# Optimization experiments

Measured on AMD Instinct MI355X. Metric: run time of the kernel, lower is better.

The kernel has to match this reference:

```python
import jax, jax.numpy as jnp
import numpy as np

INPUT_DIM = 512
NUM_CLASSES = 1000


def setup_inputs() -> dict:
    key = jax.random.key(0)
    kx, kw, kb = jax.random.split(key, 3)
    x = jax.random.normal(kx, (16384, INPUT_DIM), dtype=jnp.float32)
    # Stacked per-class Linear(input_dim, 2) params: W [C, 2, D], b [C, 2]
    lim = 1.0 / np.sqrt(INPUT_DIM)
    W = jax.random.uniform(kw, (NUM_CLASSES, 2, INPUT_DIM), dtype=jnp.float32, minval=-lim, maxval=lim)
    b = jax.random.uniform(kb, (NUM_CLASSES, 2), dtype=jnp.float32, minval=-lim, maxval=lim)
    return {"x": x, "W": W, "b": b}


def reference(x, W, b):
    # logits[b, c, t] = x[b, :] @ W[c, t, :] + b[c, t]
    logits = jnp.einsum("bd,ctd->bct", x, W) + b[None, :, :]  # [B, C, 2]
    # LogSoftmax over the 2 logits per class (torch dim=1 of the [B,2] slice)
    return jax.nn.log_softmax(logits, axis=-1)
```

## Files before the change

### kernel.cpp

```cpp
#include <hip/hip_runtime.h>
#include <cstdint>
#include <cstddef>

typedef unsigned short u16;
typedef unsigned int u32;
typedef __bf16 bf16x8 __attribute__((ext_vector_type(8)));
typedef float f32x4 __attribute__((ext_vector_type(4)));
typedef float f32x2 __attribute__((ext_vector_type(2)));

#define M_TOT 16384
#define C_TOT 1000
#define N_PAD 1024
#define K_TOT 512
#define OUT_STRIDE 2000
#define BM 128
#define BN 128
#define BK 32
#define NT 16
#define NWG 1024

__device__ __forceinline__ u16 f2bf(float f) {
  u32 u = __float_as_uint(f);
  u = (u + 0x7FFFu + ((u >> 16) & 1u)) >> 16;
  return (u16)u;
}

__global__ __launch_bounds__(256) void prep_kernel(const float* __restrict__ x,
                                                   const float* __restrict__ W,
                                                   const float* __restrict__ b,
                                                   u16* __restrict__ xb,
                                                   u16* __restrict__ wd,
                                                   float* __restrict__ bd) {
  if (blockIdx.x < 4096) {
    const int i = blockIdx.x * 256 + threadIdx.x;
    const float4* s = (const float4*)x;
    float4 a = s[2 * i], c = s[2 * i + 1];
    ushort4 r0, r1;
    r0.x = f2bf(a.x); r0.y = f2bf(a.y); r0.z = f2bf(a.z); r0.w = f2bf(a.w);
    r1.x = f2bf(c.x); r1.y = f2bf(c.y); r1.z = f2bf(c.z); r1.w = f2bf(c.w);
    ushort4* d = (ushort4*)xb;
    d[2 * i] = r0;
    d[2 * i + 1] = r1;
  } else {
    const int i = (blockIdx.x - 4096) * 256 + threadIdx.x;
    const int c = i >> 6;
    const int seg = i & 63;
    ushort4 r0 = {0, 0, 0, 0}, r1 = {0, 0, 0, 0};
    if (c < C_TOT) {
      const float4* w0 = (const float4*)(W + (size_t)(2 * c) * K_TOT) + seg * 2;
      const float4* w1 = (const float4*)(W + (size_t)(2 * c + 1) * K_TOT) + seg * 2;
      float4 a0 = w0[0], a1 = w0[1], c0 = w1[0], c1 = w1[1];
      r0.x = f2bf(a0.x - c0.x); r0.y = f2bf(a0.y - c0.y);
      r0.z = f2bf(a0.z - c0.z); r0.w = f2bf(a0.w - c0.w);
      r1.x = f2bf(a1.x - c1.x); r1.y = f2bf(a1.y - c1.y);
      r1.z = f2bf(a1.z - c1.z); r1.w = f2bf(a1.w - c1.w);
      if (seg == 0) bd[c] = b[2 * c] - b[2 * c + 1];
    } else if (seg == 0) {
      bd[c] = 0.0f;
    }
    ushort4* d = (ushort4*)(wd + (size_t)c * K_TOT);
    d[seg * 2] = r0;
    d[seg * 2 + 1] = r1;
  }
}

__device__ __forceinline__ void gload_lds(const u16* g, u16* l) {
  __builtin_amdgcn_global_load_lds((const __attribute__((address_space(1))) u32*)g,
                                   (__attribute__((address_space(3))) u32*)l, 16, 0, 0);
}

__device__ __forceinline__ void stage8k(const u16* __restrict__ gbase,
                                        u16* lb, int tid) {
#pragma unroll
  for (int i = 0; i < 2; ++i) {
    const int g = i * 256 + tid;
    const int lrow = g >> 3;
    const int u = (g & 7) ^ (lrow & 7);
    const int r = lrow | ((u >> 2) << 6);
    const int q = u & 3;
    gload_lds(gbase + (size_t)r * K_TOT + q * 8, lb + (size_t)g * 8);
  }
}

#define VMW(N) asm volatile("s_waitcnt vmcnt(" #N ")" ::: "memory")
#define CFENCE asm volatile("" ::: "memory")

__global__ __launch_bounds__(256, 2) void gemm_ls_kernel(const u16* __restrict__ A,
                                                         const u16* __restrict__ B,
                                                         const float* __restrict__ bdiff,
                                                         float* __restrict__ out) {
  __shared__ u16 As[4][4096];
  __shared__ u16 Bs[4][4096];

  const int tid = threadIdx.x;
  const int lane = tid & 63;
  const int w = tid >> 6;
  const int wm = w >> 1;
  const int wn = w & 1;

  const int bid = blockIdx.x;
  const int wg = (bid & 7) * (NWG / 8) + (bid >> 3);
  const int m0 = (wg >> 3) * BM;
  const int n0 = (wg & 7) * BN;

  const u16* gA = A + (size_t)m0 * K_TOT;
  const u16* gB = B + (size_t)n0 * K_TOT;

  const int ar = lane & 15;
  const int kq4 = lane >> 4;
  int offA[4], offB[4];
#pragma unroll
  for (int i = 0; i < 4; ++i) {
    int r = wm * 64 + i * 16 + ar;
    offA[i] = (r & 63) * 128 + (((((r >> 6) << 2) | kq4) ^ (r & 7)) << 4);
    r = wn * 64 + i * 16 + ar;
    offB[i] = (r & 63) * 128 + (((((r >> 6) << 2) | kq4) ^ (r & 7)) << 4);
  }

  f32x4 acc[4][4] = {};

#define STAGEAB(t)                                   \
  do {                                               \
    const int _b = (t) & 3;                          \
    stage8k(gA + (t) * BK, &As[_b][0], tid);         \
    stage8k(gB + (t) * BK, &Bs[_b][0], tid);         \
  } while (0)

#define COMPUTE(cb)                                                         \
  do {                                                                      \
    bf16x8 af[4], bf[4];                                                    \
    _Pragma("unroll") for (int i = 0; i < 4; ++i)                           \
        af[i] = *(const bf16x8*)((const char*)&As[(cb)][0] + offA[i]);      \
    _Pragma("unroll") for (int i = 0; i < 4; ++i)                           \
        bf[i] = *(const bf16x8*)((const char*)&Bs[(cb)][0] + offB[i]);      \
    _Pragma("unroll") for (int mi = 0; mi < 4; ++mi)                        \
        _Pragma("unroll") for (int ni = 0; ni < 4; ++ni)                    \
            acc[mi][ni] = __builtin_amdgcn_mfma_f32_16x16x32_bf16(          \
                af[mi], bf[ni], acc[mi][ni], 0, 0, 0);                      \
  } while (0)

  STAGEAB(0);
  STAGEAB(1);
  STAGEAB(2);

  for (int t = 0; t < 14; ++t) {
    VMW(8);
    __builtin_amdgcn_s_barrier();
    CFENCE;
    if (t < 13) STAGEAB(t + 3);
    COMPUTE(t & 3);
  }
  VMW(4);
  __builtin_amdgcn_s_barrier();
  CFENCE;
  COMPUTE(2);
  VMW(0);
  __builtin_amdgcn_s_barrier();
  CFENCE;
  COMPUTE(3);

  const int rbase = m0 + wm * 64 + (lane >> 4) * 4;
  const bool full = (n0 + BN <= C_TOT);

#pragma unroll
  for (int ni = 0; ni < 4; ++ni) {
    const int n = n0 + wn * 64 + ni * 16 + ar;
    if (full || n < C_TOT) {
      const float bd_r = bdiff[n];
#pragma unroll
      for (int mi = 0; mi < 4; ++mi) {
#pragma unroll
        for (int j = 0; j < 4; ++j) {
          const float d = acc[mi][ni][j] + bd_r;
          const float o0 = fminf(d, 0.0f) - __logf(1.0f + __expf(-fabsf(d)));
          const int row = rbase + mi * 16 + j;
          f32x2 v;
          v.x = o0;
          v.y = o0 - d;
          *(f32x2*)(out + (size_t)row * OUT_STRIDE + 2 * n) = v;
        }
      }
    }
  }
#undef STAGEAB
#undef COMPUTE
}

__global__ __launch_bounds__(256) void naive_kernel(const float* __restrict__ x,
                                                    const float* __restrict__ W,
                                                    const float* __restrict__ b,
                                                    float* __restrict__ out) {
  __shared__ float xs[K_TOT];
  const int row = blockIdx.x;
  for (int i = threadIdx.x; i < K_TOT; i += 256) xs[i] = x[(size_t)row * K_TOT + i];
  __syncthreads();
  for (int c = threadIdx.x; c < C_TOT; c += 256) {
    const float* w0 = W + (size_t)c * 1024;
    float l0 = b[c * 2], l1 = b[c * 2 + 1];
    for (int k = 0; k < K_TOT; ++k) {
      const float xv = xs[k];
      l0 += xv * w0[k];
      l1 += xv * w0[K_TOT + k];
    }
    const float d = l0 - l1;
    const float t = __logf(1.0f + __expf(-fabsf(d)));
    out[(size_t)row * OUT_STRIDE + c * 2]     = fminf(d, 0.0f) - t;
    out[(size_t)row * OUT_STRIDE + c * 2 + 1] = fminf(-d, 0.0f) - t;
  }
}

extern "C" void kernel_launch(void* const* d_in, const int* in_sizes, int n_in,
                              void* d_out, int out_size, void* d_ws, size_t ws_size,
                              hipStream_t stream) {
  const float* x = (const float*)d_in[0];
  const float* W = (const float*)d_in[1];
  const float* b = (const float*)d_in[2];
  float* out = (float*)d_out;

  const size_t nx = (size_t)M_TOT * K_TOT;
  const size_t nwd = (size_t)N_PAD * K_TOT;
  const size_t need = (nx + nwd) * sizeof(u16) + N_PAD * sizeof(float);

  if (ws_size < need) {
    naive_kernel<<<M_TOT, 256, 0, stream>>>(x, W, b, out);
    return;
  }

  u16* xb = (u16*)d_ws;
  u16* wd = xb + nx;
  float* bd = (float*)(wd + nwd);

  prep_kernel<<<4096 + 256, 256, 0, stream>>>(x, W, b, xb, wd, bd);
  gemm_ls_kernel<<<NWG, 256, 0, stream>>>(xb, wd, bd, out);
}
```

Before: 52.25 us.

## Fuse x fp32-to-bf16 conversion into GEMM A-tile staging via registers

Drops the separate pass that converted all of x to bf16 in workspace. The GEMM now loads fp32 x rows into registers three tiles ahead, packs them to bf16 with v_cvt_pk_bf16_f32 and writes them into swizzled LDS, while B still uses direct global-to-LDS loads. This avoids a full write and re-read of the bf16 copy of x and one kernel launch. In exchange each workgroup reads fp32 A, which is twice the bytes per tile, uses more registers for the prefetch buffers, and adds an LDS write plus lgkmcnt wait each step; s_setprio is raised around the MFMA block.

```diff
diff --git a/kernel.cpp b/kernel.cpp
--- a/kernel.cpp
+++ b/kernel.cpp
@@ -7,6 +7,7 @@
 typedef __bf16 bf16x8 __attribute__((ext_vector_type(8)));
 typedef float f32x4 __attribute__((ext_vector_type(4)));
 typedef float f32x2 __attribute__((ext_vector_type(2)));
+typedef u32 u32x4 __attribute__((ext_vector_type(4)));
 
 #define M_TOT 16384
 #define C_TOT 1000
@@ -25,43 +26,35 @@
   return (u16)u;
 }
 
-__global__ __launch_bounds__(256) void prep_kernel(const float* __restrict__ x,
-                                                   const float* __restrict__ W,
-                                                   const float* __restrict__ b,
-                                                   u16* __restrict__ xb,
-                                                   u16* __restrict__ wd,
-                                                   float* __restrict__ bd) {
-  if (blockIdx.x < 4096) {
-    const int i = blockIdx.x * 256 + threadIdx.x;
-    const float4* s = (const float4*)x;
-    float4 a = s[2 * i], c = s[2 * i + 1];
-    ushort4 r0, r1;
-    r0.x = f2bf(a.x); r0.y = f2bf(a.y); r0.z = f2bf(a.z); r0.w = f2bf(a.w);
-    r1.x = f2bf(c.x); r1.y = f2bf(c.y); r1.z = f2bf(c.z); r1.w = f2bf(c.w);
-    ushort4* d = (ushort4*)xb;
-    d[2 * i] = r0;
-    d[2 * i + 1] = r1;
-  } else {
-    const int i = (blockIdx.x - 4096) * 256 + threadIdx.x;
-    const int c = i >> 6;
-    const int seg = i & 63;
-    ushort4 r0 = {0, 0, 0, 0}, r1 = {0, 0, 0, 0};
-    if (c < C_TOT) {
-      const float4* w0 = (const float4*)(W + (size_t)(2 * c) * K_TOT) + seg * 2;
-      const float4* w1 = (const float4*)(W + (size_t)(2 * c + 1) * K_TOT) + seg * 2;
-      float4 a0 = w0[0], a1 = w0[1], c0 = w1[0], c1 = w1[1];
-      r0.x = f2bf(a0.x - c0.x); r0.y = f2bf(a0.y - c0.y);
-      r0.z = f2bf(a0.z - c0.z); r0.w = f2bf(a0.w - c0.w);
-      r1.x = f2bf(a1.x - c1.x); r1.y = f2bf(a1.y - c1.y);
-      r1.z = f2bf(a1.z - c1.z); r1.w = f2bf(a1.w - c1.w);
-      if (seg == 0) bd[c] = b[2 * c] - b[2 * c + 1];
-    } else if (seg == 0) {
-      bd[c] = 0.0f;
-    }
-    ushort4* d = (ushort4*)(wd + (size_t)c * K_TOT);
-    d[seg * 2] = r0;
-    d[seg * 2 + 1] = r1;
-  }
+__device__ __forceinline__ u32 cvtpk(float lo, float hi) {
+  u32 d;
+  asm("v_cvt_pk_bf16_f32 %0, %1, %2" : "=v"(d) : "v"(lo), "v"(hi));
+  return d;
+}
+
+__global__ __launch_bounds__(256) void wprep_kernel(const float* __restrict__ W,
+                                                    const float* __restrict__ b,
+                                                    u16* __restrict__ wd,
+                                                    float* __restrict__ bd) {
+  const int i = blockIdx.x * 256 + threadIdx.x;
+  const int c = i >> 6;
+  const int seg = i & 63;
+  ushort4 r0 = {0, 0, 0, 0}, r1 = {0, 0, 0, 0};
+  if (c < C_TOT) {
+    const float4* w0 = (const float4*)(W + (size_t)(2 * c) * K_TOT) + seg * 2;
+    const float4* w1 = (const float4*)(W + (size_t)(2 * c + 1) * K_TOT) + seg * 2;
+    float4 a0 = w0[0], a1 = w0[1], c0 = w1[0], c1 = w1[1];
+    r0.x = f2bf(a0.x - c0.x); r0.y = f2bf(a0.y - c0.y);
+    r0.z = f2bf(a0.z - c0.z); r0.w = f2bf(a0.w - c0.w);
+    r1.x = f2bf(a1.x - c1.x); r1.y = f2bf(a1.y - c1.y);
+    r1.z = f2bf(a1.z - c1.z); r1.w = f2bf(a1.w - c1.w);
+    if (seg == 0) bd[c] = b[2 * c] - b[2 * c + 1];
+  } else if (seg == 0) {
+    bd[c] = 0.0f;
+  }
+  ushort4* d = (ushort4*)(wd + (size_t)c * K_TOT);
+  d[seg * 2] = r0;
+  d[seg * 2 + 1] = r1;
 }
 
 __device__ __forceinline__ void gload_lds(const u16* g, u16* l) {
@@ -85,7 +78,7 @@
 #define VMW(N) asm volatile("s_waitcnt vmcnt(" #N ")" ::: "memory")
 #define CFENCE asm volatile("" ::: "memory")
 
-__global__ __launch_bounds__(256, 2) void gemm_ls_kernel(const u16* __restrict__ A,
+__global__ __launch_bounds__(256, 2) void gemm_ls_kernel(const float* __restrict__ Af,
                                                          const u16* __restrict__ B,
                                                          const float* __restrict__ bdiff,
                                                          float* __restrict__ out) {
@@ -103,8 +96,16 @@
   const int m0 = (wg >> 3) * BM;
   const int n0 = (wg & 7) * BN;
 
-  const u16* gA = A + (size_t)m0 * K_TOT;
+  const float* gAf = Af + (size_t)m0 * K_TOT;
   const u16* gB = B + (size_t)n0 * K_TOT;
+
+  const int lrow0 = tid >> 3;
+  const int au = (tid & 7) ^ (lrow0 & 7);
+  const int qA = au & 3;
+  const int rA0 = lrow0 | ((au >> 2) << 6);
+  const int rA1 = (32 + lrow0) | ((au >> 2) << 6);
+  const f32x4* gq0 = (const f32x4*)gAf + (size_t)rA0 * 128 + qA * 2;
+  const f32x4* gq1 = (const f32x4*)gAf + (size_t)rA1 * 128 + qA * 2;
 
   const int ar = lane & 15;
   const int kq4 = lane >> 4;
@@ -118,46 +119,69 @@
   }
 
   f32x4 acc[4][4] = {};
-
-#define STAGEAB(t)                                   \
-  do {                                               \
-    const int _b = (t) & 3;                          \
-    stage8k(gA + (t) * BK, &As[_b][0], tid);         \
-    stage8k(gB + (t) * BK, &Bs[_b][0], tid);         \
-  } while (0)
-
-#define COMPUTE(cb)                                                         \
+  f32x4 areg[3][4];
+
+#define ALOAD(T)                                   \
+  do {                                             \
+    areg[(T) % 3][0] = gq0[(T) * 8];               \
+    areg[(T) % 3][1] = gq0[(T) * 8 + 1];           \
+    areg[(T) % 3][2] = gq1[(T) * 8];               \
+    areg[(T) % 3][3] = gq1[(T) * 8 + 1];           \
+  } while (0)
+
+#define ACVT_WR(T)                                                        \
+  do {                                                                    \
+    u32x4 w0, w1;                                                         \
+    w0.x = cvtpk(areg[(T) % 3][0].x, areg[(T) % 3][0].y);                 \
+    w0.y = cvtpk(areg[(T) % 3][0].z, areg[(T) % 3][0].w);                 \
+    w0.z = cvtpk(areg[(T) % 3][1].x, areg[(T) % 3][1].y);                 \
+    w0.w = cvtpk(areg[(T) % 3][1].z, areg[(T) % 3][1].w);                 \
+    w1.x = cvtpk(areg[(T) % 3][2].x, areg[(T) % 3][2].y);                 \
+    w1.y = cvtpk(areg[(T) % 3][2].z, areg[(T) % 3][2].w);                 \
+    w1.z = cvtpk(areg[(T) % 3][3].x, areg[(T) % 3][3].y);                 \
+    w1.w = cvtpk(areg[(T) % 3][3].z, areg[(T) % 3][3].w);                 \
+    *(u32x4*)(&As[(T) & 3][(size_t)tid * 8]) = w0;                        \
+    *(u32x4*)(&As[(T) & 3][(size_t)(256 + tid) * 8]) = w1;                \
+  } while (0)
+
+#define BSTAGE(T) stage8k(gB + (T) * BK, &Bs[(T) & 3][0], tid)
+
+#define COMPUTE(T)                                                          \
   do {                                                                      \
     bf16x8 af[4], bf[4];                                                    \
     _Pragma("unroll") for (int i = 0; i < 4; ++i)                           \
-        af[i] = *(const bf16x8*)((const char*)&As[(cb)][0] + offA[i]);      \
+        af[i] = *(const bf16x8*)((const char*)&As[(T) & 3][0] + offA[i]);   \
     _Pragma("unroll") for (int i = 0; i < 4; ++i)                           \
-        bf[i] = *(const bf16x8*)((const char*)&Bs[(cb)][0] + offB[i]);      \
+        bf[i] = *(const bf16x8*)((const char*)&Bs[(T) & 3][0] + offB[i]);   \
     _Pragma("unroll") for (int mi = 0; mi < 4; ++mi)                        \
         _Pragma("unroll") for (int ni = 0; ni < 4; ++ni)                    \
             acc[mi][ni] = __builtin_amdgcn_mfma_f32_16x16x32_bf16(          \
                 af[mi], bf[ni], acc[mi][ni], 0, 0, 0);                      \
   } while (0)
 
-  STAGEAB(0);
-  STAGEAB(1);
-  STAGEAB(2);
-
-  for (int t = 0; t < 14; ++t) {
-    VMW(8);
-    __builtin_amdgcn_s_barrier();
-    CFENCE;
-    if (t < 13) STAGEAB(t + 3);
-    COMPUTE(t & 3);
-  }
-  VMW(4);
-  __builtin_amdgcn_s_barrier();
-  CFENCE;
-  COMPUTE(2);
-  VMW(0);
-  __builtin_amdgcn_s_barrier();
-  CFENCE;
-  COMPUTE(3);
+#define STEP(T, VMN)                                         \
+  do {                                                       \
+    VMW(VMN);                                                \
+    CFENCE;                                                  \
+    ACVT_WR(T);                                              \
+    if ((T) + 3 < NT) ALOAD((T) + 3);                        \
+    asm volatile("s_waitcnt lgkmcnt(0)" ::: "memory");       \
+    __builtin_amdgcn_s_barrier();                            \
+    CFENCE;                                                  \
+    if ((T) + 3 < NT) BSTAGE((T) + 3);                       \
+    __builtin_amdgcn_s_setprio(1);                           \
+    COMPUTE(T);                                              \
+    __builtin_amdgcn_s_setprio(0);                           \
+  } while (0)
+
+  ALOAD(0); BSTAGE(0);
+  ALOAD(1); BSTAGE(1);
+  ALOAD(2); BSTAGE(2);
+
+  STEP(0, 12);  STEP(1, 12);  STEP(2, 12);  STEP(3, 12);
+  STEP(4, 12);  STEP(5, 12);  STEP(6, 12);  STEP(7, 12);
+  STEP(8, 12);  STEP(9, 12);  STEP(10, 12); STEP(11, 12);
+  STEP(12, 12); STEP(13, 12); STEP(14, 6);  STEP(15, 0);
 
   const int rbase = m0 + wm * 64 + (lane >> 4) * 4;
   const bool full = (n0 + BN <= C_TOT);
@@ -182,8 +206,11 @@
       }
     }
   }
-#undef STAGEAB
+#undef ALOAD
+#undef ACVT_WR
+#undef BSTAGE
 #undef COMPUTE
+#undef STEP
 }
 
 __global__ __launch_bounds__(256) void naive_kernel(const float* __restrict__ x,
@@ -217,19 +244,17 @@
   const float* b = (const float*)d_in[2];
   float* out = (float*)d_out;
 
-  const size_t nx = (size_t)M_TOT * K_TOT;
   const size_t nwd = (size_t)N_PAD * K_TOT;
-  const size_t need = (nx + nwd) * sizeof(u16) + N_PAD * sizeof(float);
+  const size_t need = nwd * sizeof(u16) + N_PAD * sizeof(float);
 
   if (ws_size < need) {
     naive_kernel<<<M_TOT, 256, 0, stream>>>(x, W, b, out);
     return;
   }
 
-  u16* xb = (u16*)d_ws;
-  u16* wd = xb + nx;
+  u16* wd = (u16*)d_ws;
   float* bd = (float*)(wd + nwd);
 
-  prep_kernel<<<4096 + 256, 256, 0, stream>>>(x, W, b, xb, wd, bd);
-  gemm_ls_kernel<<<NWG, 256, 0, stream>>>(xb, wd, bd, out);
-}
+  wprep_kernel<<<256, 256, 0, stream>>>(W, b, wd, bd);
+  gemm_ls_kernel<<<NWG, 256, 0, stream>>>(x, wd, bd, out);
+}
```

Result: faster. 50.91 us (-2.6%).
